# Performance work log

Measured on AMD Instinct MI355X. Metric: run time of the kernel, lower is better.

## Reference

```python
import jax, jax.numpy as jnp
import numpy as np

B, C, H, W = 64, 3, 384, 384
P = 16                      # patch_size
E = 768                     # embed_dim
NH, NW = H // P, W // P     # 24, 24
N = NH * NW                 # 576 patches


def setup_inputs() -> dict:
    key = jax.random.key(0)
    k_x, k_y, k_xs, k_w, k_b = jax.random.split(key, 5)
    x = jax.random.normal(k_x, (B, C, H, W), dtype=jnp.float32)
    ys = jax.random.randint(k_y, (B, N), 0, W - P, dtype=jnp.int32)
    xs = jax.random.randint(k_xs, (B, N), 0, W - P, dtype=jnp.int32)
    # Conv2d(in_chans, embed_dim, kernel=P, stride=P) parameters
    w = jax.random.normal(k_w, (E, C, P, P), dtype=jnp.float32) * 0.02
    b = jax.random.normal(k_b, (E,), dtype=jnp.float32) * 0.02
    return {"x": x, "ys": ys, "xs": xs, "w": w, "b": b}


def _gather_patches(x, ys, xs):
    # x: [B,C,H,W]; ys/xs: [B,N] top-left corners -> patches [B,N,C,P,P]
    def one_img(img, ys_b, xs_b):
        def one_patch(y, x0):
            return jax.lax.dynamic_slice(img, (0, y, x0), (C, P, P))
        return jax.vmap(one_patch)(ys_b, xs_b)
    return jax.vmap(one_img)(x, ys, xs)


def reference(x, ys, xs, w, b):
    # patch_positions, as in the torch module
    patch_positions = jnp.stack([ys, xs], axis=-1)          # [B,N,2]
    patches = _gather_patches(x, ys, xs)                    # [B,N,C,P,P]
    # Restitched image fed to a stride-P conv == per-patch projection.
    # Conv windows exactly coincide with the restitched patches, so the
    # patch_embed is a single contraction per patch (same math, one pass).
    tokens = jnp.einsum('bncpq,ecpq->bne', patches, w) + b  # [B,N,E]
    return tokens, patch_positions
```

## Files before the change

### kernel.cpp

```cpp
#include <hip/hip_runtime.h>

#define B_    64
#define C_    3
#define H_    384
#define W_    384
#define P_    16
#define E_    768
#define N_    576
#define M_    (B_ * N_)
#define K_    (C_ * P_ * P_)
#define HW_   (H_ * W_)
#define CHW_  (C_ * H_ * W_)

#define BM    128
#define BN    128
#define BK    64
#define KITERS (K_ / BK)

typedef __attribute__((ext_vector_type(8))) short  short8;
typedef __attribute__((ext_vector_type(4))) float  f32x4;

__device__ __forceinline__ unsigned int rnepair(float a, float b) {
    unsigned ua = __float_as_uint(a), ub = __float_as_uint(b);
    ua += 0x7FFFu + ((ua >> 16) & 1u);
    ub += 0x7FFFu + ((ub >> 16) & 1u);
    return (ua >> 16) | (ub & 0xFFFF0000u);
}

__device__ __forceinline__ float4 ld16u(const float* p) {
    float4 v;
    __builtin_memcpy(&v, p, 16);
    return v;
}

__device__ __forceinline__ void gload_lds16(const void* g, void* l) {
    __builtin_amdgcn_global_load_lds(
        (const __attribute__((address_space(1))) unsigned int*)g,
        (__attribute__((address_space(3))) unsigned int*)l,
        16, 0, 0);
}

__global__ __launch_bounds__(256)
void wconv_kernel(const float* __restrict__ w, unsigned short* __restrict__ Wb)
{
    const unsigned g = blockIdx.x * 256 + threadIdx.x;
    float4 f = ((const float4*)w)[g];
    uint2 pk;
    pk.x = rnepair(f.x, f.y);
    pk.y = rnepair(f.z, f.w);
    *(uint2*)(Wb + (size_t)g * 4) = pk;
}

__global__ __launch_bounds__(256)
void fused_gemm(const float* __restrict__ x,
                const int*   __restrict__ ys,
                const int*   __restrict__ xs,
                const unsigned short* __restrict__ Wb,
                const float* __restrict__ bias,
                float*       __restrict__ out)
{
    __shared__ __align__(16) unsigned short Asm[BM * BK];
    __shared__ __align__(16) unsigned short Bsm[BN * BK];

    const int t    = threadIdx.x;
    const int wave = t >> 6;
    const int lane = t & 63;

    const int b   = blockIdx.x;
    const int xcd = b & 7;
    const int idx = b >> 3;
    const int mt  = xcd * 36 + idx / 6;
    const int et  = idx % 6;
    const int m0  = mt * BM;
    const int e0  = et * BN;

    const int p  = t >> 1;
    const int h  = t & 1;
    const int gp = m0 + p;
    const int bimg  = gp / N_;
    const int pbase = bimg * CHW_ + ys[gp] * W_ + xs[gp];
    const float* xrow = x + pbase + 2 * h * W_;

    char* aw = (char*)Asm + p * 128;
    const int awz = (p & 7) << 4;
    const int h64 = h * 64;

    const int r8 = lane >> 3;
    const int c8 = (lane & 7) * 8;
    const unsigned short* Bg = Wb + (size_t)(e0 + wave * 32 + r8) * K_ + c8;
    unsigned short* Bl = &Bsm[(wave * 32 + r8) * BK + c8];

    const int wr   = (wave >> 1) * 64;
    const int wc   = (wave & 1) * 64;
    const int lm   = lane & 15;
    const int quad = lane >> 4;
    const char* Ard = (const char*)Asm + (wr + lm) * 128;
    const int rswz = (lm & 7) << 4;

    f32x4 acc[4][4];
#pragma unroll
    for (int i = 0; i < 4; ++i)
#pragma unroll
        for (int j = 0; j < 4; ++j)
            acc[i][j] = (f32x4){0.f, 0.f, 0.f, 0.f};

    float4 fr[8];
#pragma unroll
    for (int m = 0; m < 4; ++m) fr[m]     = ld16u(xrow + 4 * m);
#pragma unroll
    for (int m = 0; m < 4; ++m) fr[4 + m] = ld16u(xrow + W_ + 4 * m);

#pragma unroll 1
    for (int it = 0; it < KITERS; ++it) {
        const unsigned short* bg = Bg + it * BK;
#pragma unroll
        for (int inst = 0; inst < 4; ++inst)
            gload_lds16(bg + (size_t)(inst * 8) * K_, Bl + inst * 8 * BK);

#pragma unroll
        for (int j = 0; j < 4; ++j) {
            uint4 wv;
            wv.x = rnepair(fr[2*j].x,   fr[2*j].y);
            wv.y = rnepair(fr[2*j].z,   fr[2*j].w);
            wv.z = rnepair(fr[2*j+1].x, fr[2*j+1].y);
            wv.w = rnepair(fr[2*j+1].z, fr[2*j+1].w);
            *(uint4*)(aw + ((h64 + j * 16) ^ awz)) = wv;
        }

        __syncthreads();

        if (it + 1 < KITERS) {
            const int itn = it + 1;
            const float* rp = xrow + (itn >> 2) * HW_ + ((itn & 3) << 2) * W_;
#pragma unroll
            for (int m = 0; m < 4; ++m) fr[m]     = ld16u(rp + 4 * m);
#pragma unroll
            for (int m = 0; m < 4; ++m) fr[4 + m] = ld16u(rp + W_ + 4 * m);
        }

#pragma unroll
        for (int s = 0; s < 2; ++s) {
            short8 af[4], bfr[4];
#pragma unroll
            for (int i = 0; i < 4; ++i)
                af[i] = *(const short8*)(Ard + i * (16 * 128)
                                             + ((s * 64 + quad * 16) ^ rswz));
#pragma unroll
            for (int j = 0; j < 4; ++j)
                bfr[j] = *(const short8*)&Bsm[(wc + j * 16 + lm) * BK + s * 32 + quad * 8];
#pragma unroll
            for (int i = 0; i < 4; ++i)
#pragma unroll
                for (int j = 0; j < 4; ++j)
                    acc[i][j] = __builtin_amdgcn_mfma_f32_16x16x32_bf16(af[i], bfr[j], acc[i][j], 0, 0, 0);
        }

        __syncthreads();
    }

    float bv[4];
#pragma unroll
    for (int j = 0; j < 4; ++j) bv[j] = bias[e0 + wc + j * 16 + lm];

#pragma unroll
    for (int i = 0; i < 4; ++i) {
#pragma unroll
        for (int j = 0; j < 4; ++j) {
            const int eo = e0 + wc + j * 16 + lm;
#pragma unroll
            for (int r = 0; r < 4; ++r) {
                const int mo = m0 + wr + i * 16 + quad * 4 + r;
                out[(size_t)mo * E_ + eo] = acc[i][j][r] + bv[j];
            }
        }
    }
}

__global__ void pos_kernel(const int* __restrict__ ys, const int* __restrict__ xs,
                           float* __restrict__ outp)
{
    int i = blockIdx.x * blockDim.x + threadIdx.x;
    if (i < M_) {
        outp[2 * i]     = (float)ys[i];
        outp[2 * i + 1] = (float)xs[i];
    }
}

extern "C" void kernel_launch(void* const* d_in, const int* in_sizes, int n_in,
                              void* d_out, int out_size, void* d_ws, size_t ws_size,
                              hipStream_t stream)
{
    const float* x    = (const float*)d_in[0];
    const int*   ys   = (const int*)d_in[1];
    const int*   xs   = (const int*)d_in[2];
    const float* w    = (const float*)d_in[3];
    const float* bias = (const float*)d_in[4];
    float* out = (float*)d_out;

    unsigned short* Wb = (unsigned short*)d_ws;

    wconv_kernel<<<(E_ * K_ / 4) / 256, 256, 0, stream>>>(w, Wb);

    fused_gemm<<<(M_ / BM) * (E_ / BN), 256, 0, stream>>>(x, ys, xs, Wb, bias, out);

    float* outp = out + (size_t)M_ * E_;
    pos_kernel<<<(M_ + 255) / 256, 256, 0, stream>>>(ys, xs, outp);
}
```

Measured before the change: 304.6 us.

## Register-prefetch B tiles with swizzled LDS and reorder loads for overlap

```diff
diff --git a/kernel.cpp b/kernel.cpp
--- a/kernel.cpp
+++ b/kernel.cpp
@@ -33,13 +33,6 @@
     return v;
 }
 
-__device__ __forceinline__ void gload_lds16(const void* g, void* l) {
-    __builtin_amdgcn_global_load_lds(
-        (const __attribute__((address_space(1))) unsigned int*)g,
-        (__attribute__((address_space(3))) unsigned int*)l,
-        16, 0, 0);
-}
-
 __global__ __launch_bounds__(256)
 void wconv_kernel(const float* __restrict__ w, unsigned short* __restrict__ Wb)
 {
@@ -51,7 +44,7 @@
     *(uint2*)(Wb + (size_t)g * 4) = pk;
 }
 
-__global__ __launch_bounds__(256)
+__global__ __launch_bounds__(256, 3)
 void fused_gemm(const float* __restrict__ x,
                 const int*   __restrict__ ys,
                 const int*   __restrict__ xs,
@@ -77,24 +70,22 @@
     const int p  = t >> 1;
     const int h  = t & 1;
     const int gp = m0 + p;
-    const int bimg  = gp / N_;
-    const int pbase = bimg * CHW_ + ys[gp] * W_ + xs[gp];
-    const float* xrow = x + pbase + 2 * h * W_;
-
+    const int bimg = gp / N_;
+    const float* xrow = x + (size_t)bimg * CHW_ + ys[gp] * W_ + xs[gp] + 2 * h * W_;
     char* aw = (char*)Asm + p * 128;
     const int awz = (p & 7) << 4;
     const int h64 = h * 64;
 
     const int r8 = lane >> 3;
-    const int c8 = (lane & 7) * 8;
-    const unsigned short* Bg = Wb + (size_t)(e0 + wave * 32 + r8) * K_ + c8;
-    unsigned short* Bl = &Bsm[(wave * 32 + r8) * BK + c8];
+    const unsigned short* Bg = Wb + (size_t)(e0 + wave * 32 + r8) * K_ + (lane & 7) * 8;
+    char* bw = (char*)Bsm + (wave * 32 + r8) * 128 + (((lane & 7) * 16) ^ (r8 << 4));
 
     const int wr   = (wave >> 1) * 64;
     const int wc   = (wave & 1) * 64;
     const int lm   = lane & 15;
     const int quad = lane >> 4;
     const char* Ard = (const char*)Asm + (wr + lm) * 128;
+    const char* Brd = (const char*)Bsm + (wc + lm) * 128;
     const int rswz = (lm & 7) << 4;
 
     f32x4 acc[4][4];
@@ -109,13 +100,23 @@
     for (int m = 0; m < 4; ++m) fr[m]     = ld16u(xrow + 4 * m);
 #pragma unroll
     for (int m = 0; m < 4; ++m) fr[4 + m] = ld16u(xrow + W_ + 4 * m);
-
-#pragma unroll 1
+    uint4 bq[4];
+#pragma unroll
+    for (int i2 = 0; i2 < 4; ++i2)
+        bq[i2] = *(const uint4*)(Bg + (size_t)i2 * 8 * K_);
+
+#pragma unroll 2
     for (int it = 0; it < KITERS; ++it) {
-        const unsigned short* bg = Bg + it * BK;
-#pragma unroll
-        for (int inst = 0; inst < 4; ++inst)
-            gload_lds16(bg + (size_t)(inst * 8) * K_, Bl + inst * 8 * BK);
+        float4 nfr[8];
+        if (it + 1 < KITERS) {
+            const int itn = it + 1;
+            const float* rp = xrow + (itn >> 2) * HW_ + ((itn & 3) << 2) * W_;
+#pragma unroll
+            for (int m = 0; m < 4; ++m) nfr[m]     = ld16u(rp + 4 * m);
+#pragma unroll
+            for (int m = 0; m < 4; ++m) nfr[4 + m] = ld16u(rp + W_ + 4 * m);
+        }
+        __builtin_amdgcn_sched_barrier(0);
 
 #pragma unroll
         for (int j = 0; j < 4; ++j) {
@@ -126,28 +127,33 @@
             wv.w = rnepair(fr[2*j+1].z, fr[2*j+1].w);
             *(uint4*)(aw + ((h64 + j * 16) ^ awz)) = wv;
         }
-
-        __syncthreads();
+#pragma unroll
+        for (int i2 = 0; i2 < 4; ++i2)
+            *(uint4*)(bw + i2 * (8 * 128)) = bq[i2];
+
+        asm volatile("s_waitcnt lgkmcnt(0)" ::: "memory");
+        __builtin_amdgcn_s_barrier();
+        __builtin_amdgcn_sched_barrier(0);
 
         if (it + 1 < KITERS) {
-            const int itn = it + 1;
-            const float* rp = xrow + (itn >> 2) * HW_ + ((itn & 3) << 2) * W_;
-#pragma unroll
-            for (int m = 0; m < 4; ++m) fr[m]     = ld16u(rp + 4 * m);
-#pragma unroll
-            for (int m = 0; m < 4; ++m) fr[4 + m] = ld16u(rp + W_ + 4 * m);
-        }
+            const unsigned short* bgn = Bg + (it + 1) * BK;
+#pragma unroll
+            for (int i2 = 0; i2 < 4; ++i2)
+                bq[i2] = *(const uint4*)(bgn + (size_t)i2 * 8 * K_);
+        }
+        __builtin_amdgcn_sched_barrier(0);
 
 #pragma unroll
         for (int s = 0; s < 2; ++s) {
             short8 af[4], bfr[4];
 #pragma unroll
             for (int i = 0; i < 4; ++i)
-                af[i] = *(const short8*)(Ard + i * (16 * 128)
-                                             + ((s * 64 + quad * 16) ^ rswz));
+                af[i]  = *(const short8*)(Ard + i * (16 * 128)
+                                              + ((s * 64 + quad * 16) ^ rswz));
 #pragma unroll
             for (int j = 0; j < 4; ++j)
-                bfr[j] = *(const short8*)&Bsm[(wc + j * 16 + lm) * BK + s * 32 + quad * 8];
+                bfr[j] = *(const short8*)(Brd + j * (16 * 128)
+                                              + ((s * 64 + quad * 16) ^ rswz));
 #pragma unroll
             for (int i = 0; i < 4; ++i)
 #pragma unroll
@@ -155,7 +161,14 @@
                     acc[i][j] = __builtin_amdgcn_mfma_f32_16x16x32_bf16(af[i], bfr[j], acc[i][j], 0, 0, 0);
         }
 
-        __syncthreads();
+        asm volatile("" ::: "memory");
+        __builtin_amdgcn_s_barrier();
+        __builtin_amdgcn_sched_barrier(0);
+
+        if (it + 1 < KITERS) {
+#pragma unroll
+            for (int m = 0; m < 8; ++m) fr[m] = nfr[m];
+        }
     }
 
     float bv[4];
```

Measured after the change: 478.0 us. 1.57x slower.
